# Kernel optimization log

Measured on AMD Instinct MI355X. Metric: run time of the kernel, lower is better.

Reference implementation:

```python
import jax, jax.numpy as jnp
import numpy as np

B, N, CIN, H, E = 1, 20000, 128, 128, 320000


def setup_inputs() -> dict:
    key = jax.random.key(0)
    ks = jax.random.split(key, 16)
    x = jax.random.normal(ks[0], (B, N, CIN), jnp.float32)
    edge_index = jax.random.randint(ks[1], (2, E), 0, N, dtype=jnp.int64)
    edge_weight = jax.random.uniform(ks[2], (E,), jnp.float32)
    h = jax.random.normal(ks[3], (B, N, H), jnp.float32)
    c = jax.random.normal(ks[4], (B, N, H), jnp.float32)
    # GCN stack params, gate order [i, f, c, o]; 2 layers each (K=2)
    Wx0 = jax.random.normal(ks[5], (4, CIN, H), jnp.float32) / np.float32(np.sqrt(CIN))
    bx0 = jnp.zeros((4, H), jnp.float32)
    Wx1 = jax.random.normal(ks[6], (4, H, H), jnp.float32) / np.float32(np.sqrt(H))
    bx1 = jnp.zeros((4, H), jnp.float32)
    Wh0 = jax.random.normal(ks[7], (4, H, H), jnp.float32) / np.float32(np.sqrt(H))
    bh0 = jnp.zeros((4, H), jnp.float32)
    Wh1 = jax.random.normal(ks[8], (4, H, H), jnp.float32) / np.float32(np.sqrt(H))
    bh1 = jnp.zeros((4, H), jnp.float32)
    wc = jax.random.normal(ks[9], (3, H), jnp.float32) * 0.1  # peephole [i, f, o]
    bg = jnp.zeros((4, H), jnp.float32)  # gate biases [i, f, c, o]
    return dict(x=x, edge_index=edge_index, edge_weight=edge_weight, h=h, c=c,
                Wx0=Wx0, bx0=bx0, Wx1=Wx1, bx1=bx1,
                Wh0=Wh0, bh0=bh0, Wh1=Wh1, bh1=bh1, wc=wc, bg=bg)


def reference(x, edge_index, edge_weight, h, c,
              Wx0, bx0, Wx1, bx1, Wh0, bh0, Wh1, bh1, wc, bg):
    n = x.shape[1]
    src, dst = edge_index[0], edge_index[1]
    loop = jnp.arange(n)
    src2 = jnp.concatenate([src, loop])
    dst2 = jnp.concatenate([dst, loop])
    w2 = jnp.concatenate([edge_weight, jnp.ones((n,), edge_weight.dtype)])
    deg = jax.ops.segment_sum(w2, dst2, num_segments=n)
    dis = jnp.where(deg > 0, jax.lax.rsqrt(jnp.maximum(deg, 1e-12)), 0.0)
    norm = dis[src2] * w2 * dis[dst2]  # sym GCN norm with self loops

    def prop(t):  # t: [..., N, F] -> D^-1/2 (A+I) D^-1/2 t
        lead = t.shape[:-2]
        tf = t.reshape((-1,) + t.shape[-2:])
        m = tf[:, src2, :] * norm[None, :, None]
        agg = jax.vmap(lambda mm: jax.ops.segment_sum(mm, dst2, num_segments=n))(m)
        return agg.reshape(lead + agg.shape[-2:])

    def gcn4(t, W0, b0, W1, b1):  # 2-layer GCN, 4 gates at once
        a = prop(t)  # shared first aggregation: [B,N,F]
        h0 = jax.nn.relu(jnp.einsum('bnc,gch->gbnh', a, W0) + b0[:, None, None, :])
        a1 = prop(h0)  # [4,B,N,H]
        return jnp.einsum('gbnh,ghk->gbnk', a1, W1) + b1[:, None, None, :]

    G = gcn4(x, Wx0, bx0, Wx1, bx1) + gcn4(h, Wh0, bh0, Wh1, bh1)  # [4,B,N,H]
    I = jax.nn.sigmoid(G[0] + wc[0] * c + bg[0])
    F = jax.nn.sigmoid(G[1] + wc[1] * c + bg[1])
    T = jnp.tanh(G[2] + bg[2])
    Cn = F * c + I * T
    O = jax.nn.sigmoid(G[3] + wc[2] * Cn + bg[3])
    Hn = O * jnp.tanh(Cn)
    return (Hn, Cn)
```

## Files before the change

### kernel.cpp

```cpp
#include <hip/hip_runtime.h>
#include <hip/hip_bf16.h>
#include <stdint.h>

#define NN    20000
#define NP    20096
#define EE    320000
#define CH    128
#define GC    512
#define NHtot 2560000

typedef short bf16x8 __attribute__((ext_vector_type(8)));
typedef float f32x4  __attribute__((ext_vector_type(4)));

__device__ __forceinline__ float bf2f(unsigned short u) {
    union { unsigned int i; float f; } c; c.i = ((unsigned int)u) << 16; return c.f;
}
__device__ __forceinline__ unsigned short f2bf(float f) {
    __hip_bfloat16 b = __float2bfloat16(f);
    union { __hip_bfloat16 b; unsigned short u; } c; c.b = b; return c.u;
}
__device__ __forceinline__ void fma8(uint4 u, float n, float* acc) {
    union { unsigned int i; float f; } t;
    t.i = u.x << 16;         acc[0] += n * t.f;
    t.i = u.x & 0xffff0000u; acc[1] += n * t.f;
    t.i = u.y << 16;         acc[2] += n * t.f;
    t.i = u.y & 0xffff0000u; acc[3] += n * t.f;
    t.i = u.z << 16;         acc[4] += n * t.f;
    t.i = u.z & 0xffff0000u; acc[5] += n * t.f;
    t.i = u.w << 16;         acc[6] += n * t.f;
    t.i = u.w & 0xffff0000u; acc[7] += n * t.f;
}
__device__ __forceinline__ void fma4(uint2 u, float n, float* acc) {
    union { unsigned int i; float f; } t;
    t.i = u.x << 16;         acc[0] += n * t.f;
    t.i = u.x & 0xffff0000u; acc[1] += n * t.f;
    t.i = u.y << 16;         acc[2] += n * t.f;
    t.i = u.y & 0xffff0000u; acc[3] += n * t.f;
}
__device__ __forceinline__ void tof8(uint4 u, float* f) {
    union { unsigned int i; float f; } t;
    t.i = u.x << 16;         f[0] = t.f;
    t.i = u.x & 0xffff0000u; f[1] = t.f;
    t.i = u.y << 16;         f[2] = t.f;
    t.i = u.y & 0xffff0000u; f[3] = t.f;
    t.i = u.z << 16;         f[4] = t.f;
    t.i = u.z & 0xffff0000u; f[5] = t.f;
    t.i = u.w << 16;         f[6] = t.f;
    t.i = u.w & 0xffff0000u; f[7] = t.f;
}
__device__ __forceinline__ void tof4(uint2 u, float* f) {
    union { unsigned int i; float f; } t;
    t.i = u.x << 16;         f[0] = t.f;
    t.i = u.x & 0xffff0000u; f[1] = t.f;
    t.i = u.y << 16;         f[2] = t.f;
    t.i = u.y & 0xffff0000u; f[3] = t.f;
}
__device__ __forceinline__ uint2 pack4(const float* f) {
    uint2 v;
    v.x = (unsigned int)f2bf(f[0]) | ((unsigned int)f2bf(f[1]) << 16);
    v.y = (unsigned int)f2bf(f[2]) | ((unsigned int)f2bf(f[3]) << 16);
    return v;
}

__global__ void k_count(const int* __restrict__ ei, int* __restrict__ cnt) {
    int e = blockIdx.x * 256 + threadIdx.x;
    if (e >= EE) return;
    atomicAdd(&cnt[ei[EE + e]], 1);
}

__global__ void k_scan1(const int* __restrict__ cnt, int* __restrict__ rowoff,
                        int* __restrict__ bsum) {
    __shared__ int wsum[4];
    int i = blockIdx.x * 256 + threadIdx.x;
    int self = (i < NN) ? cnt[i] : 0;
    int lane = threadIdx.x & 63, wid = threadIdx.x >> 6;
    int v = self;
    #pragma unroll
    for (int off = 1; off < 64; off <<= 1) {
        int u = __shfl_up(v, off);
        if (lane >= off) v += u;
    }
    if (lane == 63) wsum[wid] = v;
    __syncthreads();
    int wof = 0;
    for (int k = 0; k < wid; ++k) wof += wsum[k];
    if (i < NN) rowoff[i] = wof + v - self;
    if (threadIdx.x == 255) bsum[blockIdx.x] = wof + v;
}

__global__ void k_scan2(int* __restrict__ bsum) {
    int lane = threadIdx.x;
    int base = 0;
    for (int start = 0; start < 80; start += 64) {
        int i = start + lane;
        int self = (i < 80) ? bsum[i] : 0;
        int v = self;
        #pragma unroll
        for (int off = 1; off < 64; off <<= 1) {
            int u = __shfl_up(v, off);
            if (lane >= off) v += u;
        }
        if (i < 80) bsum[i] = base + v - self;
        base += __shfl(v, 63);
    }
}

__global__ void k_scan3(int* __restrict__ rowoff, const int* __restrict__ bsum,
                        int* __restrict__ cur) {
    int i = blockIdx.x * 256 + threadIdx.x;
    if (i < NN) {
        int v = rowoff[i] + bsum[i >> 8];
        rowoff[i] = v; cur[i] = v;
    }
    if (i == NN) rowoff[NN] = EE;
}

__global__ void k_scatter(const int* __restrict__ ei, const float* __restrict__ ew,
                          int* __restrict__ cur,
                          int* __restrict__ csrs, float* __restrict__ csrw) {
    int e = blockIdx.x * 256 + threadIdx.x;
    if (e >= EE) return;
    int s = ei[e], d = ei[EE + e];
    int p = atomicAdd(&cur[d], 1);
    csrs[p] = s; csrw[p] = ew[e];
}

__global__ __launch_bounds__(256) void k_degcast(
        const float* __restrict__ x, const float* __restrict__ h,
        const int* __restrict__ rowoff, const float* __restrict__ csrw,
        float* __restrict__ dis, unsigned short* __restrict__ xhb) {
    int wid = threadIdx.x >> 6, lane = threadIdx.x & 63;
    int w = blockIdx.x * 4 + wid;
    int e0 = rowoff[w], e1 = rowoff[w + 1];
    float s = 0.f;
    for (int e = e0 + lane; e < e1; e += 64) s += csrw[e];
    #pragma unroll
    for (int off = 32; off; off >>= 1) s += __shfl_xor(s, off);
    float dn = rsqrtf(fmaxf(1.0f + s, 1e-12f));
    if (lane == 0) dis[w] = dn;
    const float* src = (lane < 32) ? x + (size_t)w * CH + lane * 4
                                   : h + (size_t)w * CH + (lane - 32) * 4;
    float4 v = *(const float4*)src;
    float f[4] = { dn * v.x, dn * v.y, dn * v.z, dn * v.w };
    *(uint2*)(xhb + (size_t)w * 256 + lane * 4) = pack4(f);
}

__global__ void k_prepw(const float* __restrict__ W0, const float* __restrict__ W1,
                        const float* __restrict__ W2, const float* __restrict__ W3,
                        unsigned short* __restrict__ T0, unsigned short* __restrict__ T1,
                        unsigned short* __restrict__ T2, unsigned short* __restrict__ T3,
                        const float* __restrict__ bx1, const float* __restrict__ bh1,
                        const float* __restrict__ bg, float* __restrict__ btot) {
    if (blockIdx.z == 0 && blockIdx.y == 0 && blockIdx.x < 2) {
        int f = blockIdx.x * 256 + threadIdx.x;
        btot[f] = bx1[f] + bh1[f] + bg[f];
    }
    const float* W; unsigned short* T;
    switch (blockIdx.z) {
        case 0:  W = W0; T = T0; break;
        case 1:  W = W1; T = T1; break;
        case 2:  W = W2; T = T2; break;
        default: W = W3; T = T3; break;
    }
    int g = blockIdx.y;
    int n = blockIdx.x * 2 + (threadIdx.x >> 7);
    int k = threadIdx.x & 127;
    T[((size_t)g * 128 + n) * 128 + k] = f2bf(W[((size_t)g * 128 + k) * 128 + n]);
}

__global__ __launch_bounds__(256) void k_prop256(
        const unsigned short* __restrict__ tab, unsigned short* __restrict__ o,
        const int* __restrict__ rowoff, const int* __restrict__ csrs,
        const float* __restrict__ csrw, const float* __restrict__ dis) {
    int w = blockIdx.x * 4 + (threadIdx.x >> 6);
    int lane = threadIdx.x & 63;
    const uint2* T2 = (const uint2*)tab;
    float acc[4];
    tof4(T2[(size_t)w * 64 + lane], acc);
    int e = rowoff[w], e1 = rowoff[w + 1];
    for (; e + 4 <= e1; e += 4) {
        int   s0 = csrs[e],   s1 = csrs[e+1], s2 = csrs[e+2], s3 = csrs[e+3];
        float n0 = csrw[e],   n1 = csrw[e+1], n2 = csrw[e+2], n3 = csrw[e+3];
        uint2 u0 = T2[(size_t)s0 * 64 + lane];
        uint2 u1 = T2[(size_t)s1 * 64 + lane];
        uint2 u2 = T2[(size_t)s2 * 64 + lane];
        uint2 u3 = T2[(size_t)s3 * 64 + lane];
        fma4(u0, n0, acc); fma4(u1, n1, acc); fma4(u2, n2, acc); fma4(u3, n3, acc);
    }
    for (; e < e1; ++e) {
        fma4(T2[(size_t)csrs[e] * 64 + lane], csrw[e], acc);
    }
    float dw = dis[w];
    #pragma unroll
    for (int j = 0; j < 4; ++j) acc[j] *= dw;
    ((uint2*)o)[(size_t)w * 64 + lane] = pack4(acc);
}

#define SWZ(r, c8) (((r) << 4) + ((c8) ^ ((r) & 15)))

__global__ __launch_bounds__(256) void k_gemm1(
        const unsigned short* __restrict__ A,
        const unsigned short* __restrict__ Wtx, const unsigned short* __restrict__ Wth,
        const float* __restrict__ bx0, const float* __restrict__ bh0,
        unsigned short* __restrict__ outx, unsigned short* __restrict__ outh) {
    __shared__ uint4 As[2048];
    __shared__ uint4 Bs[2048];
    const int side = blockIdx.z;
    const int aoff = side * 128;
    const unsigned short* Wt = side ? Wth : Wtx;
    const float* bias        = side ? bh0 : bx0;
    unsigned short* out      = side ? outh : outx;

    const int    g    = blockIdx.y;
    const size_t row0 = (size_t)blockIdx.x * 128;
    const int    t    = threadIdx.x;

    #pragma unroll
    for (int p = 0; p < 8; ++p) {
        int id = t + 256 * p, r = id >> 4, c8 = id & 15;
        As[SWZ(r, c8)] = *(const uint4*)(A + (row0 + r) * 256 + aoff + c8 * 8);
    }
    const unsigned short* Wg = Wt + (size_t)g * 16384;
    #pragma unroll
    for (int p = 0; p < 8; ++p) {
        int id = t + 256 * p, r = id >> 4, c8 = id & 15;
        Bs[SWZ(r, c8)] = *(const uint4*)(Wg + r * CH + c8 * 8);
    }
    __syncthreads();

    const int wid = t >> 6, l = t & 63;
    const int m0 = (wid >> 1) * 64, n0 = (wid & 1) * 64;
    const int lm = l & 15, q = l >> 4;
    f32x4 acc[4][4];
    #pragma unroll
    for (int i = 0; i < 4; ++i)
        #pragma unroll
        for (int j = 0; j < 4; ++j) { acc[i][j][0]=0.f; acc[i][j][1]=0.f; acc[i][j][2]=0.f; acc[i][j][3]=0.f; }

    #pragma unroll
    for (int kc = 0; kc < 4; ++kc) {
        int c8 = kc * 4 + q;
        bf16x8 a[4], b[4];
        #pragma unroll
        for (int i = 0; i < 4; ++i) { int r = m0 + i * 16 + lm; a[i] = *(const bf16x8*)&As[SWZ(r, c8)]; }
        #pragma unroll
        for (int j = 0; j < 4; ++j) { int r = n0 + j * 16 + lm; b[j] = *(const bf16x8*)&Bs[SWZ(r, c8)]; }
        #pragma unroll
        for (int i = 0; i < 4; ++i)
            #pragma unroll
            for (int j = 0; j < 4; ++j)
                acc[i][j] = __builtin_amdgcn_mfma_f32_16x16x32_bf16(a[i], b[j], acc[i][j], 0, 0, 0);
    }

    #pragma unroll
    for (int j = 0; j < 4; ++j) {
        float bb = bias[g * CH + n0 + j * 16 + lm];
        #pragma unroll
        for (int i = 0; i < 4; ++i)
            #pragma unroll
            for (int r = 0; r < 4; ++r) {
                int rowl = m0 + i * 16 + q * 4 + r;
                int col  = n0 + j * 16 + lm;
                out[(row0 + rowl) * GC + g * CH + col] = f2bf(fmaxf(acc[i][j][r] + bb, 0.f));
            }
    }
}

__global__ __launch_bounds__(256) void k_gemm2(
        const unsigned short* __restrict__ A1, const unsigned short* __restrict__ A2,
        const unsigned short* __restrict__ Wt1, const unsigned short* __restrict__ Wt2,
        const float* __restrict__ dis, unsigned short* __restrict__ outS) {
    __shared__ uint4 As[2048];
    __shared__ uint4 Bs[2048];
    const int    g    = blockIdx.y;
    const size_t row0 = (size_t)blockIdx.x * 128;
    const int    t    = threadIdx.x;
    const int wid = t >> 6, l = t & 63;
    const int m0 = (wid >> 1) * 64, n0 = (wid & 1) * 64;
    const int lm = l & 15, q = l >> 4;
    f32x4 acc[4][4];
    #pragma unroll
    for (int i = 0; i < 4; ++i)
        #pragma unroll
        for (int j = 0; j < 4; ++j) { acc[i][j][0]=0.f; acc[i][j][1]=0.f; acc[i][j][2]=0.f; acc[i][j][3]=0.f; }

    for (int side = 0; side < 2; ++side) {
        if (side) __syncthreads();
        const unsigned short* Ap = side ? A2 : A1;
        const unsigned short* Wg = (side ? Wt2 : Wt1) + (size_t)g * 16384;
        #pragma unroll
        for (int p = 0; p < 8; ++p) {
            int id = t + 256 * p, r = id >> 4, c8 = id & 15;
            As[SWZ(r, c8)] = *(const uint4*)(Ap + (row0 + r) * GC + g * CH + c8 * 8);
        }
        #pragma unroll
        for (int p = 0; p < 8; ++p) {
            int id = t + 256 * p, r = id >> 4, c8 = id & 15;
            Bs[SWZ(r, c8)] = *(const uint4*)(Wg + r * CH + c8 * 8);
        }
        __syncthreads();
        #pragma unroll
        for (int kc = 0; kc < 4; ++kc) {
            int c8 = kc * 4 + q;
            bf16x8 a[4], b[4];
            #pragma unroll
            for (int i = 0; i < 4; ++i) { int r = m0 + i * 16 + lm; a[i] = *(const bf16x8*)&As[SWZ(r, c8)]; }
            #pragma unroll
            for (int j = 0; j < 4; ++j) { int r = n0 + j * 16 + lm; b[j] = *(const bf16x8*)&Bs[SWZ(r, c8)]; }
            #pragma unroll
            for (int i = 0; i < 4; ++i)
                #pragma unroll
                for (int j = 0; j < 4; ++j)
                    acc[i][j] = __builtin_amdgcn_mfma_f32_16x16x32_bf16(a[i], b[j], acc[i][j], 0, 0, 0);
        }
    }

    #pragma unroll
    for (int j = 0; j < 4; ++j)
        #pragma unroll
        for (int i = 0; i < 4; ++i)
            #pragma unroll
            for (int r = 0; r < 4; ++r) {
                int rowl = m0 + i * 16 + q * 4 + r;
                int col  = n0 + j * 16 + lm;
                float dr = dis[row0 + rowl];
                outS[(row0 + rowl) * GC + g * CH + col] = f2bf(dr * acc[i][j][r]);
            }
}

#define GIDX(f) ((f) + ((f) >> 5))
__global__ __launch_bounds__(256) void k_prop512g(
        const unsigned short* __restrict__ Sb, float* __restrict__ out,
        const int* __restrict__ rowoff, const int* __restrict__ csrs,
        const float* __restrict__ csrw, const float* __restrict__ dis,
        const float* __restrict__ c, const float* __restrict__ btot,
        const float* __restrict__ wc) {
    __shared__ float gbuf[4][528];
    int wid  = threadIdx.x >> 6, lane = threadIdx.x & 63;
    int w    = blockIdx.x * 4 + wid;
    const uint4* S4 = (const uint4*)Sb;
    float acc[8];
    tof8(S4[(size_t)w * 64 + lane], acc);
    int e = rowoff[w], e1 = rowoff[w + 1];
    for (; e + 4 <= e1; e += 4) {
        int   s0 = csrs[e],   s1 = csrs[e+1], s2 = csrs[e+2], s3 = csrs[e+3];
        float n0 = csrw[e],   n1 = csrw[e+1], n2 = csrw[e+2], n3 = csrw[e+3];
        uint4 u0 = S4[(size_t)s0 * 64 + lane];
        uint4 u1 = S4[(size_t)s1 * 64 + lane];
        uint4 u2 = S4[(size_t)s2 * 64 + lane];
        uint4 u3 = S4[(size_t)s3 * 64 + lane];
        fma8(u0, n0, acc); fma8(u1, n1, acc); fma8(u2, n2, acc); fma8(u3, n3, acc);
    }
    for (; e < e1; ++e) {
        fma8(S4[(size_t)csrs[e] * 64 + lane], csrw[e], acc);
    }
    float dw = dis[w];
    #pragma unroll
    for (int j = 0; j < 8; ++j) {
        int f = lane * 8 + j;
        gbuf[wid][GIDX(f)] = dw * acc[j];
    }
    __syncthreads();
    const float* gb = gbuf[wid];
    #pragma unroll
    for (int t2 = 0; t2 < 2; ++t2) {
        int hh = lane + 64 * t2;
        float g0 = gb[GIDX(hh)]       + btot[hh];
        float g1 = gb[GIDX(128 + hh)] + btot[128 + hh];
        float g2 = gb[GIDX(256 + hh)] + btot[256 + hh];
        float g3 = gb[GIDX(384 + hh)] + btot[384 + hh];
        float cv = c[(size_t)w * CH + hh];
        float I  = 1.f / (1.f + expf(-(g0 + wc[hh]       * cv)));
        float F  = 1.f / (1.f + expf(-(g1 + wc[128 + hh] * cv)));
        float T  = tanhf(g2);
        float Cn = F * cv + I * T;
        float O  = 1.f / (1.f + expf(-(g3 + wc[256 + hh] * Cn)));
        out[(size_t)w * CH + hh]         = O * tanhf(Cn);
        out[NHtot + (size_t)w * CH + hh] = Cn;
    }
}

extern "C" void kernel_launch(void* const* d_in, const int* in_sizes, int n_in,
                              void* d_out, int out_size, void* d_ws, size_t ws_size,
                              hipStream_t stream) {
    (void)in_sizes; (void)n_in; (void)out_size; (void)ws_size;
    const float* x   = (const float*)d_in[0];
    const int*   ei  = (const int*)d_in[1];
    const float* ew  = (const float*)d_in[2];
    const float* h   = (const float*)d_in[3];
    const float* c   = (const float*)d_in[4];
    const float* Wx0 = (const float*)d_in[5];
    const float* bx0 = (const float*)d_in[6];
    const float* Wx1 = (const float*)d_in[7];
    const float* bx1 = (const float*)d_in[8];
    const float* Wh0 = (const float*)d_in[9];
    const float* bh0 = (const float*)d_in[10];
    const float* Wh1 = (const float*)d_in[11];
    const float* bh1 = (const float*)d_in[12];
    const float* wc  = (const float*)d_in[13];
    const float* bg  = (const float*)d_in[14];
    float* out = (float*)d_out;

    float* wsf  = (float*)d_ws;
    float* dis  = wsf;
    int*   cnt  = (int*)(wsf + 20480);
    int*   row  = (int*)(wsf + 40960);
    int*   cur  = (int*)(wsf + 61696);
    int*   bsum = (int*)(wsf + 82176);
    float* btot = wsf + 82432;
    int*   csrs = (int*)(wsf + 82944);
    float* csrw = wsf + 402944;
    unsigned short* Wt0x = (unsigned short*)(wsf + 722944);
    unsigned short* Wt0h = (unsigned short*)(wsf + 755712);
    unsigned short* Wt1x = (unsigned short*)(wsf + 788480);
    unsigned short* Wt1h = (unsigned short*)(wsf + 821248);
    unsigned short* xhb  = (unsigned short*)(wsf + 854016);
    unsigned short* axh  = (unsigned short*)(wsf + 3426304);
    unsigned short* h0x  = (unsigned short*)(wsf + 5998592);
    unsigned short* h0h  = (unsigned short*)(wsf + 11143168);
    unsigned short* Sb   = (unsigned short*)(wsf + 16287744);

    hipMemsetAsync(cnt, 0, 20480 * sizeof(int), stream);

    k_count  <<<EE / 256, 256, 0, stream>>>(ei, cnt);
    k_scan1  <<<80, 256, 0, stream>>>(cnt, row, bsum);
    k_scan2  <<<1, 64, 0, stream>>>(bsum);
    k_scan3  <<<80, 256, 0, stream>>>(row, bsum, cur);
    k_scatter<<<EE / 256, 256, 0, stream>>>(ei, ew, cur, csrs, csrw);

    dim3 pw(64, 4, 4);
    k_prepw  <<<pw, 256, 0, stream>>>(Wx0, Wh0, Wx1, Wh1, Wt0x, Wt0h, Wt1x, Wt1h,
                                      bx1, bh1, bg, btot);
    k_degcast<<<NN / 4, 256, 0, stream>>>(x, h, row, csrw, dis, xhb);

    k_prop256<<<NN / 4, 256, 0, stream>>>(xhb, axh, row, csrs, csrw, dis);

    dim3 g1(NP / 128, 4, 2);
    k_gemm1<<<g1, 256, 0, stream>>>(axh, Wt0x, Wt0h, bx0, bh0, h0x, h0h);
    dim3 g2(NP / 128, 4);
    k_gemm2<<<g2, 256, 0, stream>>>(h0x, h0h, Wt1x, Wt1h, dis, Sb);

    k_prop512g<<<NN / 4, 256, 0, stream>>>(Sb, out, row, csrs, csrw, dis, c, btot, wc);
}
```

Measured before the change: 259.7 us.

## Merge count and weight prep kernels; use two waves per node in final propagation

Folds the edge-count atomic kernel and the weight transpose/bias prep kernel into one launch, removing one kernel dispatch. Shrinks the first propagation blocks from 4 to 2 waves. Reworks the final 512-feature propagation so each node is handled by a 128-thread block of two waves, each gathering 8-byte slices instead of 16-byte slices. This gives more waves per node and a simpler gate epilogue with one thread per hidden unit, at the cost of more, smaller gather requests and more blocks.

```diff
diff --git a/kernel.cpp b/kernel.cpp
--- a/kernel.cpp
+++ b/kernel.cpp
@@ -12,23 +12,9 @@
 typedef short bf16x8 __attribute__((ext_vector_type(8)));
 typedef float f32x4  __attribute__((ext_vector_type(4)));
 
-__device__ __forceinline__ float bf2f(unsigned short u) {
-    union { unsigned int i; float f; } c; c.i = ((unsigned int)u) << 16; return c.f;
-}
 __device__ __forceinline__ unsigned short f2bf(float f) {
     __hip_bfloat16 b = __float2bfloat16(f);
     union { __hip_bfloat16 b; unsigned short u; } c; c.b = b; return c.u;
-}
-__device__ __forceinline__ void fma8(uint4 u, float n, float* acc) {
-    union { unsigned int i; float f; } t;
-    t.i = u.x << 16;         acc[0] += n * t.f;
-    t.i = u.x & 0xffff0000u; acc[1] += n * t.f;
-    t.i = u.y << 16;         acc[2] += n * t.f;
-    t.i = u.y & 0xffff0000u; acc[3] += n * t.f;
-    t.i = u.z << 16;         acc[4] += n * t.f;
-    t.i = u.z & 0xffff0000u; acc[5] += n * t.f;
-    t.i = u.w << 16;         acc[6] += n * t.f;
-    t.i = u.w & 0xffff0000u; acc[7] += n * t.f;
 }
 __device__ __forceinline__ void fma4(uint2 u, float n, float* acc) {
     union { unsigned int i; float f; } t;
@@ -37,17 +23,6 @@
     t.i = u.y << 16;         acc[2] += n * t.f;
     t.i = u.y & 0xffff0000u; acc[3] += n * t.f;
 }
-__device__ __forceinline__ void tof8(uint4 u, float* f) {
-    union { unsigned int i; float f; } t;
-    t.i = u.x << 16;         f[0] = t.f;
-    t.i = u.x & 0xffff0000u; f[1] = t.f;
-    t.i = u.y << 16;         f[2] = t.f;
-    t.i = u.y & 0xffff0000u; f[3] = t.f;
-    t.i = u.z << 16;         f[4] = t.f;
-    t.i = u.z & 0xffff0000u; f[5] = t.f;
-    t.i = u.w << 16;         f[6] = t.f;
-    t.i = u.w & 0xffff0000u; f[7] = t.f;
-}
 __device__ __forceinline__ void tof4(uint2 u, float* f) {
     union { unsigned int i; float f; } t;
     t.i = u.x << 16;         f[0] = t.f;
@@ -62,10 +37,35 @@
     return v;
 }
 
-__global__ void k_count(const int* __restrict__ ei, int* __restrict__ cnt) {
-    int e = blockIdx.x * 256 + threadIdx.x;
-    if (e >= EE) return;
-    atomicAdd(&cnt[ei[EE + e]], 1);
+__global__ void k_cntprep(const int* __restrict__ ei, int* __restrict__ cnt,
+                          const float* __restrict__ W0, const float* __restrict__ W1,
+                          const float* __restrict__ W2, const float* __restrict__ W3,
+                          unsigned short* __restrict__ T0, unsigned short* __restrict__ T1,
+                          unsigned short* __restrict__ T2, unsigned short* __restrict__ T3,
+                          const float* __restrict__ bx1, const float* __restrict__ bh1,
+                          const float* __restrict__ bg, float* __restrict__ btot) {
+    int bid = blockIdx.x;
+    if (bid < EE / 256) {
+        int e = bid * 256 + threadIdx.x;
+        atomicAdd(&cnt[ei[EE + e]], 1);
+        return;
+    }
+    int pid = bid - EE / 256;
+    int z = pid >> 8, y = (pid >> 6) & 3, xb = pid & 63;
+    if (z == 0 && y == 0 && xb < 2) {
+        int f = xb * 256 + threadIdx.x;
+        btot[f] = bx1[f] + bh1[f] + bg[f];
+    }
+    const float* W; unsigned short* T;
+    switch (z) {
+        case 0:  W = W0; T = T0; break;
+        case 1:  W = W1; T = T1; break;
+        case 2:  W = W2; T = T2; break;
+        default: W = W3; T = T3; break;
+    }
+    int n = xb * 2 + (threadIdx.x >> 7);
+    int k = threadIdx.x & 127;
+    T[((size_t)y * 128 + n) * 128 + k] = f2bf(W[((size_t)y * 128 + k) * 128 + n]);
 }
 
 __global__ void k_scan1(const int* __restrict__ cnt, int* __restrict__ rowoff,
@@ -145,34 +145,11 @@
     *(uint2*)(xhb + (size_t)w * 256 + lane * 4) = pack4(f);
 }
 
-__global__ void k_prepw(const float* __restrict__ W0, const float* __restrict__ W1,
-                        const float* __restrict__ W2, const float* __restrict__ W3,
-                        unsigned short* __restrict__ T0, unsigned short* __restrict__ T1,
-                        unsigned short* __restrict__ T2, unsigned short* __restrict__ T3,
-                        const float* __restrict__ bx1, const float* __restrict__ bh1,
-                        const float* __restrict__ bg, float* __restrict__ btot) {
-    if (blockIdx.z == 0 && blockIdx.y == 0 && blockIdx.x < 2) {
-        int f = blockIdx.x * 256 + threadIdx.x;
-        btot[f] = bx1[f] + bh1[f] + bg[f];
-    }
-    const float* W; unsigned short* T;
-    switch (blockIdx.z) {
-        case 0:  W = W0; T = T0; break;
-        case 1:  W = W1; T = T1; break;
-        case 2:  W = W2; T = T2; break;
-        default: W = W3; T = T3; break;
-    }
-    int g = blockIdx.y;
-    int n = blockIdx.x * 2 + (threadIdx.x >> 7);
-    int k = threadIdx.x & 127;
-    T[((size_t)g * 128 + n) * 128 + k] = f2bf(W[((size_t)g * 128 + k) * 128 + n]);
-}
-
-__global__ __launch_bounds__(256) void k_prop256(
+__global__ __launch_bounds__(128) void k_prop256(
         const unsigned short* __restrict__ tab, unsigned short* __restrict__ o,
         const int* __restrict__ rowoff, const int* __restrict__ csrs,
         const float* __restrict__ csrw, const float* __restrict__ dis) {
-    int w = blockIdx.x * 4 + (threadIdx.x >> 6);
+    int w = blockIdx.x * 2 + (threadIdx.x >> 6);
     int lane = threadIdx.x & 63;
     const uint2* T2 = (const uint2*)tab;
     float acc[4];
@@ -329,55 +306,52 @@
 }
 
 #define GIDX(f) ((f) + ((f) >> 5))
-__global__ __launch_bounds__(256) void k_prop512g(
+__global__ __launch_bounds__(128) void k_prop512g(
         const unsigned short* __restrict__ Sb, float* __restrict__ out,
         const int* __restrict__ rowoff, const int* __restrict__ csrs,
         const float* __restrict__ csrw, const float* __restrict__ dis,
         const float* __restrict__ c, const float* __restrict__ btot,
         const float* __restrict__ wc) {
-    __shared__ float gbuf[4][528];
-    int wid  = threadIdx.x >> 6, lane = threadIdx.x & 63;
-    int w    = blockIdx.x * 4 + wid;
-    const uint4* S4 = (const uint4*)Sb;
-    float acc[8];
-    tof8(S4[(size_t)w * 64 + lane], acc);
+    __shared__ float gbuf[528];
+    int half = threadIdx.x >> 6, lane = threadIdx.x & 63;
+    int w = blockIdx.x;
+    const uint2* S2 = (const uint2*)Sb;
+    size_t foff = (size_t)half * 64 + lane;
+    float acc[4];
+    tof4(S2[(size_t)w * 128 + foff], acc);
     int e = rowoff[w], e1 = rowoff[w + 1];
     for (; e + 4 <= e1; e += 4) {
         int   s0 = csrs[e],   s1 = csrs[e+1], s2 = csrs[e+2], s3 = csrs[e+3];
         float n0 = csrw[e],   n1 = csrw[e+1], n2 = csrw[e+2], n3 = csrw[e+3];
-        uint4 u0 = S4[(size_t)s0 * 64 + lane];
-        uint4 u1 = S4[(size_t)s1 * 64 + lane];
-        uint4 u2 = S4[(size_t)s2 * 64 + lane];
-        uint4 u3 = S4[(size_t)s3 * 64 + lane];
-        fma8(u0, n0, acc); fma8(u1, n1, acc); fma8(u2, n2, acc); fma8(u3, n3, acc);
+        uint2 u0 = S2[(size_t)s0 * 128 + foff];
+        uint2 u1 = S2[(size_t)s1 * 128 + foff];
+        uint2 u2 = S2[(size_t)s2 * 128 + foff];
+        uint2 u3 = S2[(size_t)s3 * 128 + foff];
+        fma4(u0, n0, acc); fma4(u1, n1, acc); fma4(u2, n2, acc); fma4(u3, n3, acc);
     }
     for (; e < e1; ++e) {
-        fma8(S4[(size_t)csrs[e] * 64 + lane], csrw[e], acc);
+        fma4(S2[(size_t)csrs[e] * 128 + foff], csrw[e], acc);
     }
     float dw = dis[w];
     #pragma unroll
-    for (int j = 0; j < 8; ++j) {
-        int f = lane * 8 + j;
-        gbuf[wid][GIDX(f)] = dw * acc[j];
+    for (int j = 0; j < 4; ++j) {
+        int f = half * 256 + lane * 4 + j;
+        gbuf[GIDX(f)] = dw * acc[j];
     }
     __syncthreads();
-    const float* gb = gbuf[wid];
-    #pragma unroll
-    for (int t2 = 0; t2 < 2; ++t2) {
-        int hh = lane + 64 * t2;
-        float g0 = gb[GIDX(hh)]       + btot[hh];
-        float g1 = gb[GIDX(128 + hh)] + btot[128 + hh];
-        float g2 = gb[GIDX(256 + hh)] + btot[256 + hh];
-        float g3 = gb[GIDX(384 + hh)] + btot[384 + hh];
-        float cv = c[(size_t)w * CH + hh];
-        float I  = 1.f / (1.f + expf(-(g0 + wc[hh]       * cv)));
-        float F  = 1.f / (1.f + expf(-(g1 + wc[128 + hh] * cv)));
-        float T  = tanhf(g2);
-        float Cn = F * cv + I * T;
-        float O  = 1.f / (1.f + expf(-(g3 + wc[256 + hh] * Cn)));
-        out[(size_t)w * CH + hh]         = O * tanhf(Cn);
-        out[NHtot + (size_t)w * CH + hh] = Cn;
-    }
+    int hh = threadIdx.x;
+    float g0 = gbuf[GIDX(hh)]       + btot[hh];
+    float g1 = gbuf[GIDX(128 + hh)] + btot[128 + hh];
+    float g2 = gbuf[GIDX(256 + hh)] + btot[256 + hh];
+    float g3 = gbuf[GIDX(384 + hh)] + btot[384 + hh];
+    float cv = c[(size_t)w * CH + hh];
+    float I  = 1.f / (1.f + expf(-(g0 + wc[hh]       * cv)));
+    float F  = 1.f / (1.f + expf(-(g1 + wc[128 + hh] * cv)));
+    float T  = tanhf(g2);
+    float Cn = F * cv + I * T;
+    float O  = 1.f / (1.f + expf(-(g3 + wc[256 + hh] * Cn)));
+    out[(size_t)w * CH + hh]         = O * tanhf(Cn);
+    out[NHtot + (size_t)w * CH + hh] = Cn;
 }
 
 extern "C" void kernel_launch(void* const* d_in, const int* in_sizes, int n_in,
@@ -422,23 +396,23 @@
 
     hipMemsetAsync(cnt, 0, 20480 * sizeof(int), stream);
 
-    k_count  <<<EE / 256, 256, 0, stream>>>(ei, cnt);
+    k_cntprep<<<EE / 256 + 1024, 256, 0, stream>>>(ei, cnt,
+                                                   Wx0, Wh0, Wx1, Wh1,
+                                                   Wt0x, Wt0h, Wt1x, Wt1h,
+                                                   bx1, bh1, bg, btot);
     k_scan1  <<<80, 256, 0, stream>>>(cnt, row, bsum);
     k_scan2  <<<1, 64, 0, stream>>>(bsum);
     k_scan3  <<<80, 256, 0, stream>>>(row, bsum, cur);
     k_scatter<<<EE / 256, 256, 0, stream>>>(ei, ew, cur, csrs, csrw);
 
-    dim3 pw(64, 4, 4);
-    k_prepw  <<<pw, 256, 0, stream>>>(Wx0, Wh0, Wx1, Wh1, Wt0x, Wt0h, Wt1x, Wt1h,
-                                      bx1, bh1, bg, btot);
     k_degcast<<<NN / 4, 256, 0, stream>>>(x, h, row, csrw, dis, xhb);
 
-    k_prop256<<<NN / 4, 256, 0, stream>>>(xhb, axh, row, csrs, csrw, dis);
+    k_prop256<<<NN / 2, 128, 0, stream>>>(xhb, axh, row, csrs, csrw, dis);
 
     dim3 g1(NP / 128, 4, 2);
     k_gemm1<<<g1, 256, 0, stream>>>(axh, Wt0x, Wt0h, bx0, bh0, h0x, h0h);
     dim3 g2(NP / 128, 4);
     k_gemm2<<<g2, 256, 0, stream>>>(h0x, h0h, Wt1x, Wt1h, dis, Sb);
 
-    k_prop512g<<<NN / 4, 256, 0, stream>>>(Sb, out, row, csrs, csrw, dis, c, btot, wc);
-}
+    k_prop512g<<<NN, 128, 0, stream>>>(Sb, out, row, csrs, csrw, dis, c, btot, wc);
+}
```

Result: no change. 258.1 us (-0.6%).
